# Performance work log

Measured on AMD Instinct MI355X. Metric: run time of the kernel, lower is better.

The kernel has to match this reference:

```python
import jax, jax.numpy as jnp
import numpy as np

K = 16
EPS = 1e-5

def _conv1x1(w, b, x):
    # w: [O, I], x: [B, I, N] -> [B, O, N]
    return jnp.einsum('oi,bin->bon', w, x) + b[None, :, None]

def _bn(g, be, m, v, x):
    # inference-mode batchnorm over channel dim of [B, C, N]
    inv = g / jnp.sqrt(v + EPS)
    return x * inv[None, :, None] + (be - m * inv)[None, :, None]

def setup_inputs() -> dict:
    key = jax.random.key(0)
    ks = jax.random.split(key, 16)
    B, C, N = 2, 128, 8192
    d = {}
    d['x'] = jax.random.normal(ks[0], (B, C, N), jnp.float32)
    d['xyz'] = jax.random.normal(ks[1], (B, N, 3), jnp.float32)
    def conv(k, o, i):
        k1, k2 = jax.random.split(k)
        s = 1.0 / np.sqrt(i)
        return (jax.random.uniform(k1, (o, i), jnp.float32, -s, s),
                jax.random.uniform(k2, (o,), jnp.float32, -s, s))
    def bn(k, c):
        return (jax.random.uniform(k, (c,), jnp.float32, 0.5, 1.5),
                jnp.zeros((c,), jnp.float32), jnp.zeros((c,), jnp.float32), jnp.ones((c,), jnp.float32))
    # boundary_net: 2C->C (bn,relu), C->C (bn,relu)
    d['bw1'], d['bb1'] = conv(ks[2], C, 2 * C)
    d['bn1g'], d['bn1b'], d['bn1m'], d['bn1v'] = bn(ks[3], C)
    d['bw2'], d['bb2'] = conv(ks[4], C, C)
    d['bn2g'], d['bn2b'], d['bn2m'], d['bn2v'] = bn(ks[5], C)
    # spatial_relation: 4->32 (bn,relu), 32->64
    d['sw1'], d['sb1'] = conv(ks[6], 32, 4)
    d['sbng'], d['sbnb'], d['sbnm'], d['sbnv'] = bn(ks[7], 32)
    d['sw2'], d['sb2'] = conv(ks[8], 64, 32)
    # attention: C+64 -> C//2 (bn,relu), C//2 -> C, sigmoid
    d['aw1'], d['ab1'] = conv(ks[9], C // 2, C + 64)
    d['abng'], d['abnb'], d['abnm'], d['abnv'] = bn(ks[10], C // 2)
    d['aw2'], d['ab2'] = conv(ks[11], C, C // 2)
    return d

def reference(x, xyz, bw1, bb1, bn1g, bn1b, bn1m, bn1v, bw2, bb2, bn2g, bn2b, bn2m, bn2v,
              sw1, sb1, sbng, sbnb, sbnm, sbnv, sw2, sb2,
              aw1, ab1, abng, abnb, abnm, abnv, aw2, ab2):
    B, C, N = x.shape
    # pairwise squared distances [B, N, N]
    xx = jnp.sum(xyz * xyz, axis=2)  # [B, N]
    dist = xx[:, :, None] + xx[:, None, :] - 2.0 * jnp.einsum('bnd,bmd->bnm', xyz, xyz)
    _, knn_idx = jax.lax.top_k(-dist, K)  # [B, N, K], K smallest distances
    # gather neighbor coords [B, N, K, 3]
    knn_xyz = jax.vmap(lambda p, i: p[i])(xyz, knn_idx)
    rel = knn_xyz - xyz[:, :, None, :]                  # [B, N, K, 3]
    rel_d = jnp.sqrt(jnp.sum(rel * rel, axis=-1))       # [B, N, K]
    mean_rel = jnp.mean(rel, axis=2).transpose(0, 2, 1)   # [B, 3, N]
    mean_d = jnp.mean(rel_d, axis=2)[:, None, :]           # [B, 1, N]
    spatial = jnp.concatenate([mean_rel, mean_d], axis=1)  # [B, 4, N]
    s = jax.nn.relu(_bn(sbng, sbnb, sbnm, sbnv, _conv1x1(sw1, sb1, spatial)))
    spatial_feat = _conv1x1(sw2, sb2, s)  # [B, 64, N]
    # gather neighbor features [B, C, N, K]
    knn_feat = jax.vmap(lambda xb, ib: xb[:, ib])(x, knn_idx)
    max_diff = jnp.max(knn_feat - x[:, :, :, None], axis=3)  # [B, C, N]
    bf = jnp.concatenate([x, max_diff], axis=1)  # [B, 2C, N]
    bf = jax.nn.relu(_bn(bn1g, bn1b, bn1m, bn1v, _conv1x1(bw1, bb1, bf)))
    boundary_feat = jax.nn.relu(_bn(bn2g, bn2b, bn2m, bn2v, _conv1x1(bw2, bb2, bf)))
    ai = jnp.concatenate([x, spatial_feat], axis=1)  # [B, C+64, N]
    a = jax.nn.relu(_bn(abng, abnb, abnm, abnv, _conv1x1(aw1, ab1, ai)))
    attn = jax.nn.sigmoid(_conv1x1(aw2, ab2, a))  # [B, C, N]
    return x + boundary_feat * attn
```

## Files before the change

### kernel.cpp

```cpp
#include <hip/hip_runtime.h>
#include <math.h>

#define NPTS  8192
#define NB    2
#define NTOT  (NPTS*NB)
#define GD    60
#define NCELL (GD*GD*GD)
#define TOTC  (NB*NCELL)
#define HCELL 0.2f
#define INVH  5.0f
#define ORGN  (-6.0f)
#define NN    8192
#define SCAN_CHUNK 1024
#define NBLK_SCAN  ((TOTC + SCAN_CHUNK - 1) / SCAN_CHUNK)
#define RMAX_GRID 4
#define RSTART    2
#define LIST_CAP 1024
#define SEL_CAP  1024

#define OFF_CNT     ((size_t)0)
#define OFF_OFFS    (OFF_CNT    + (size_t)TOTC*4)
#define OFF_CELLID  (OFF_OFFS   + (size_t)TOTC*4)
#define OFF_RANK    (OFF_CELLID + (size_t)NTOT*4)
#define OFF_SPOS    (OFF_RANK   + (size_t)NTOT*4)
#define OFF_KNN     (OFF_SPOS   + (size_t)NTOT*16)
#define OFF_SPATIAL (OFF_KNN    + (size_t)NTOT*16*4)
#define OFF_XT      (OFF_SPATIAL+ (size_t)NB*4*NPTS*4)
#define OFF_MD      (OFF_XT     + (size_t)NB*128*NPTS*4)
#define OFF_S1      (OFF_MD     + (size_t)NB*128*NPTS*4)
#define OFF_SF      (OFF_S1     + (size_t)NB*32*NPTS*4)
#define OFF_Y1      (OFF_SF     + (size_t)NB*64*NPTS*4)
#define OFF_Y2      (OFF_Y1     + (size_t)NB*128*NPTS*4)
#define OFF_A1      (OFF_Y2     + (size_t)NB*128*NPTS*4)
#define OFF_SC      (OFF_A1     + (size_t)NB*64*NPTS*4)
#define OFF_BSUM    (OFF_SC     + (size_t)1088*4)
#define OFF_BPRE    (OFF_BSUM   + (size_t)NBLK_SCAN*4)
#define OFF_RNG     (((OFF_BPRE + (size_t)NBLK_SCAN*4) + 15) & ~(size_t)15)

static __device__ __forceinline__ float sumsq3(float x, float y, float z) {
    return __fadd_rn(__fadd_rn(__fmul_rn(x, x), __fmul_rn(y, y)), __fmul_rn(z, z));
}
static __device__ __forceinline__ float pdist4(float qx, float qy, float qz, float qxx,
                                               float px, float py, float pz) {
    float pxx = sumsq3(px, py, pz);
    float dot = __fadd_rn(__fadd_rn(__fmul_rn(qx, px), __fmul_rn(qy, py)), __fmul_rn(qz, pz));
    return __fsub_rn(__fadd_rn(qxx, pxx), __fadd_rn(dot, dot));
}
static __device__ __forceinline__ unsigned fkey(float f) {
    unsigned b = __float_as_uint(f);
    return b ^ ((unsigned)(((int)b) >> 31) | 0x80000000u);
}
static __device__ __forceinline__ unsigned long long shflx64(unsigned long long v, int m) {
    unsigned lo = __shfl_xor((unsigned)v, m, 64);
    unsigned hi = __shfl_xor((unsigned)(v >> 32), m, 64);
    return ((unsigned long long)hi << 32) | lo;
}
static __device__ __forceinline__ int wave_scan_incl(int v, int lane) {
    #pragma unroll
    for (int d = 1; d < 64; d <<= 1) {
        int u = __shfl_up(v, d, 64);
        v += (lane >= d) ? u : 0;
    }
    return v;
}

__global__ void cell_build(const float* __restrict__ xyz, int* __restrict__ cnt,
                           int* __restrict__ cellid, int* __restrict__ rank) {
    int t = blockIdx.x * 256 + threadIdx.x;
    if (t >= NTOT) return;
    const float* p = xyz + (size_t)t * 3;
    float x = p[0], y = p[1], z = p[2];
    int cx = min(GD - 1, max(0, (int)floorf((x - ORGN) * INVH)));
    int cy = min(GD - 1, max(0, (int)floorf((y - ORGN) * INVH)));
    int cz = min(GD - 1, max(0, (int)floorf((z - ORGN) * INVH)));
    int gcell = (t >> 13) * NCELL + (cz * GD + cy) * GD + cx;
    rank[t] = atomicAdd(&cnt[gcell], 1);
    cellid[t] = gcell;
}

__global__ __launch_bounds__(256) void scan_sums(const int* __restrict__ cnt, int* __restrict__ bsum) {
    __shared__ int red[256];
    int blk = blockIdx.x, t = threadIdx.x;
    int i0 = blk * SCAN_CHUNK + t * 4;
    int s = 0;
    if (i0 + 3 < TOTC) {
        int4 v = *(const int4*)(cnt + i0);
        s = v.x + v.y + v.z + v.w;
    } else {
        for (int j = 0; j < 4; ++j) if (i0 + j < TOTC) s += cnt[i0 + j];
    }
    red[t] = s;
    __syncthreads();
    for (int d = 128; d > 0; d >>= 1) {
        if (t < d) red[t] += red[t + d];
        __syncthreads();
    }
    if (t == 0) bsum[blk] = red[0];
}

__global__ __launch_bounds__(512) void scan_top(const int* __restrict__ bsum, int* __restrict__ bpre) {
    __shared__ int ps[512];
    int t = threadIdx.x;
    int v = (t < NBLK_SCAN) ? bsum[t] : 0;
    ps[t] = v;
    __syncthreads();
    for (int d = 1; d < 512; d <<= 1) {
        int u = 0;
        if (t >= d) u = ps[t - d];
        __syncthreads();
        ps[t] += u;
        __syncthreads();
    }
    if (t < NBLK_SCAN) bpre[t] = ps[t] - v;
}

__global__ __launch_bounds__(256) void scan_write(const int* __restrict__ cnt, const int* __restrict__ bpre,
                                                  int* __restrict__ offs, int2* __restrict__ rng) {
    __shared__ int ps[256];
    int blk = blockIdx.x, t = threadIdx.x;
    int i0 = blk * SCAN_CHUNK + t * 4;
    int a = 0, b = 0, c = 0, d = 0;
    if (i0 + 3 < TOTC) {
        int4 v = *(const int4*)(cnt + i0);
        a = v.x; b = v.y; c = v.z; d = v.w;
    } else {
        if (i0 + 0 < TOTC) a = cnt[i0 + 0];
        if (i0 + 1 < TOTC) b = cnt[i0 + 1];
        if (i0 + 2 < TOTC) c = cnt[i0 + 2];
        if (i0 + 3 < TOTC) d = cnt[i0 + 3];
    }
    int s = a + b + c + d;
    ps[t] = s;
    __syncthreads();
    for (int dd = 1; dd < 256; dd <<= 1) {
        int u = 0;
        if (t >= dd) u = ps[t - dd];
        __syncthreads();
        ps[t] += u;
        __syncthreads();
    }
    int base = bpre[blk] + ps[t] - s;
    if (i0 + 3 < TOTC) {
        offs[i0 + 0] = base;
        offs[i0 + 1] = base + a;
        offs[i0 + 2] = base + a + b;
        offs[i0 + 3] = base + a + b + c;
        *(int4*)(rng + i0)     = make_int4(base, base + a, base + a, base + a + b);
        *(int4*)(rng + i0 + 2) = make_int4(base + a + b, base + a + b + c,
                                           base + a + b + c, base + s);
    } else {
        if (i0 + 0 < TOTC) { offs[i0 + 0] = base;             rng[i0 + 0] = make_int2(base, base + a); }
        if (i0 + 1 < TOTC) { offs[i0 + 1] = base + a;         rng[i0 + 1] = make_int2(base + a, base + a + b); }
        if (i0 + 2 < TOTC) { offs[i0 + 2] = base + a + b;     rng[i0 + 2] = make_int2(base + a + b, base + a + b + c); }
        if (i0 + 3 < TOTC) { offs[i0 + 3] = base + a + b + c; rng[i0 + 3] = make_int2(base + a + b + c, base + s); }
    }
}

__global__ void scatter_k(const float* __restrict__ xyz, const int* __restrict__ cellid,
                          const int* __restrict__ rank, const int* __restrict__ offs,
                          float4* __restrict__ spos) {
    int t = blockIdx.x * 256 + threadIdx.x;
    if (t >= NTOT) return;
    const float* p = xyz + (size_t)t * 3;
    float x = p[0], y = p[1], z = p[2];
    int pos = offs[cellid[t]] + rank[t];
    spos[pos] = make_float4(x, y, z, __int_as_float(t & (NPTS - 1)));
}

__global__ __launch_bounds__(64) void knn_kernel(const float4* __restrict__ spos,
                                                 const int2* __restrict__ rng,
                                                 int* __restrict__ knn,
                                                 float* __restrict__ spatial) {
    __shared__ __align__(16) char shraw[12288];
    int* lst = (int*)shraw;
    unsigned long long* sel = (unsigned long long*)(shraw + 4096);
    int lane = threadIdx.x;
    int bid  = blockIdx.x;
    int s = (bid & 7) * (NTOT / 8) + (bid >> 3);
    float4 q = spos[s];
    float qx = q.x, qy = q.y, qz = q.z;
    float qxx = sumsq3(qx, qy, qz);
    int b  = s >> 13;
    int nq = __float_as_int(q.w);
    int cx = min(GD - 1, max(0, (int)floorf((qx - ORGN) * INVH)));
    int cy = min(GD - 1, max(0, (int)floorf((qy - ORGN) * INVH)));
    int cz = min(GD - 1, max(0, (int)floorf((qz - ORGN) * INVH)));
    const int2* rg = rng + b * NCELL;

    float mlx = qx - (ORGN + (float)cx * HCELL);
    float mhx = (ORGN + (float)(cx + 1) * HCELL) - qx;
    float mly = qy - (ORGN + (float)cy * HCELL);
    float mhy = (ORGN + (float)(cy + 1) * HCELL) - qy;
    float mlz = qz - (ORGN + (float)cz * HCELL);
    float mhz = (ORGN + (float)(cz + 1) * HCELL) - qz;
    float margin0 = fminf(fminf(fminf(mlx, mhx), fminf(mly, mhy)), fminf(mlz, mhz));

    float mfin = margin0 + (float)(RMAX_GRID + 1) * HCELL;
    unsigned long long tkfin = (mfin > 0.f)
        ? ((unsigned long long)(fkey(mfin * mfin - 1e-4f) + 1u) << 27) : 0ULL;

    int tot = 0, ovf = 0;

    auto scan_runs = [&](int num, int start) {
        int rem = num, cur = start;
        for (;;) {
            int inc = wave_scan_incl(rem, lane);
            int ctot = __shfl(inc, 63, 64);
            if (ctot == 0) break;
            int excl = inc - rem;
            int space = LIST_CAP - excl;
            int take = min(rem, max(space, 0));
            for (int j = 0; j < take; ++j) lst[excl + j] = cur + j;
            rem -= take; cur += take;
            int n = min(ctot, LIST_CAP);
            asm volatile("s_waitcnt lgkmcnt(0)" ::: "memory");
            __builtin_amdgcn_sched_barrier(0);
            int sp_cur = (lane < n) ? lst[lane] : 0;
            float4 p_cur = spos[sp_cur];
            for (int t0 = 0; t0 < n; t0 += 64) {
                int tt = t0 + lane, tn = tt + 64;
                int sp_nx = (tn < n) ? lst[tn] : 0;
                float4 p_nx = spos[sp_nx];
                unsigned long long key = ~0ULL;
                if (tt < n) {
                    float d = pdist4(qx, qy, qz, qxx, p_cur.x, p_cur.y, p_cur.z);
                    key = ((unsigned long long)fkey(d) << 27)
                        | ((unsigned long long)(unsigned)__float_as_int(p_cur.w) << 14)
                        | (unsigned)sp_cur;
                }
                bool pass = (tt < n) && (key < tkfin);
                unsigned long long mk = __ballot(pass);
                int cnum = (int)__popcll(mk);
                if (tot + cnum > SEL_CAP) { ovf = 1; return; }
                if (pass) sel[tot + (int)__popcll(mk & ((1ULL << lane) - 1ULL))] = key;
                tot += cnum;
                sp_cur = sp_nx; p_cur = p_nx;
            }
            asm volatile("s_waitcnt lgkmcnt(0)" ::: "memory");
            __builtin_amdgcn_sched_barrier(0);
        }
    };

    int brute = (tkfin == 0ULL) ? 1 : 0;

    if (!brute) {
        int Lb = 2 * RSTART + 1;
        int nrows = Lb * Lb;
        int num = 0, start = 0;
        if (lane < nrows) {
            int dzr = lane / Lb - RSTART, dyr = lane % Lb - RSTART;
            int zc = cz + dzr, yc = cy + dyr;
            if ((unsigned)zc < GD && (unsigned)yc < GD) {
                int rowb = (zc * GD + yc) * GD;
                int xlo = max(cx - RSTART, 0), xhi = min(cx + RSTART, GD - 1);
                start = rg[rowb + xlo].x;
                num   = rg[rowb + xhi].y - start;
            }
        }
        scan_runs(num, start);
        if (ovf) brute = 1;
    }

    int R = RSTART;
    unsigned long long tkey_sel = ~0ULL;
    int cselq = 0;
    while (!brute) {
        float mR  = margin0 + (float)R * HCELL;
        float mR1 = mR - HCELL, mR2 = mR1 - HCELL;
        unsigned long long tk2 = (mR  > 0.f) ? ((unsigned long long)(fkey(mR  * mR  - 1e-4f) + 1u) << 27) : 0ULL;
        unsigned long long tk1 = (mR1 > 0.f) ? ((unsigned long long)(fkey(mR1 * mR1 - 1e-4f) + 1u) << 27) : 0ULL;
        unsigned long long tk0 = (mR2 > 0.f) ? ((unsigned long long)(fkey(mR2 * mR2 - 1e-4f) + 1u) << 27) : 0ULL;
        unsigned pk01 = 0; int c2 = 0;
        for (int t0 = 0; t0 < tot; t0 += 64) {
            int tt = t0 + lane;
            if (tt < tot) {
                unsigned long long v = sel[tt];
                pk01 += (v < tk0) ? 1u : 0u;
                pk01 += (v < tk1) ? 0x10000u : 0u;
                c2   += (v < tk2) ? 1 : 0;
            }
        }
        for (int o = 32; o > 0; o >>= 1) { pk01 += __shfl_xor(pk01, o, 64); c2 += __shfl_xor(c2, o, 64); }
        if (c2 >= 16) {
            int c0 = (int)(pk01 & 0xFFFFu), c1 = (int)(pk01 >> 16);
            if      (c0 >= 16) { tkey_sel = tk0; cselq = c0; }
            else if (c1 >= 16) { tkey_sel = tk1; cselq = c1; }
            else               { tkey_sel = tk2; cselq = c2; }
            break;
        }
        if (R >= RMAX_GRID) { brute = 1; break; }
        ++R;
        int Ls = 2 * R + 1;
        int P = Ls * Ls, P2 = (Ls - 2) * (Ls - 2);
        int nruns = P + P2;
        for (int r0 = 0; r0 < nruns && !ovf; r0 += 64) {
            int u = r0 + lane;
            int num = 0, start = 0;
            if (u < nruns) {
                int dzr, dyr, xlo, xhi;
                if (u < P) {
                    dzr = u / Ls - R; dyr = u % Ls - R;
                    bool outer = (dzr == -R || dzr == R || dyr == -R || dyr == R);
                    if (outer) { xlo = max(cx - R, 0); xhi = min(cx + R, GD - 1); }
                    else       { xlo = cx - R; xhi = cx - R; }
                } else {
                    int v = u - P; int L2 = Ls - 2;
                    dzr = v / L2 - (R - 1); dyr = v % L2 - (R - 1);
                    xlo = cx + R; xhi = cx + R;
                }
                int zc = cz + dzr, yc = cy + dyr;
                if ((unsigned)zc < GD && (unsigned)yc < GD && xlo >= 0 && xhi < GD) {
                    int rowb = (zc * GD + yc) * GD;
                    start = rg[rowb + xlo].x;
                    num   = rg[rowb + xhi].y - start;
                }
            }
            scan_runs(num, start);
        }
        if (ovf) brute = 1;
    }

    if (brute) {
        const float LADR[16] = {0.35f, 0.4725f, 0.637875f, 0.86113125f,
                                1.1625272f, 1.5694117f, 2.1187058f, 2.8602529f,
                                3.8613414f, 5.2128109f, 7.0372947f, 9.5003478f,
                                12.825470f, 17.314384f, 23.374418f, 31.555464f};
        int sbase = b << 13;
        int cc[16];
        #pragma unroll
        for (int k = 0; k < 16; ++k) cc[k] = 0;
        for (int i0 = 0; i0 < NPTS; i0 += 64) {
            float4 p = spos[sbase + i0 + lane];
            float d = pdist4(qx, qy, qz, qxx, p.x, p.y, p.z);
            #pragma unroll
            for (int k = 0; k < 16; ++k) cc[k] += (d < LADR[k] * LADR[k]) ? 1 : 0;
        }
        #pragma unroll
        for (int k = 0; k < 16; ++k)
            for (int o = 32; o > 0; o >>= 1) cc[k] += __shfl_xor(cc[k], o, 64);
        float Tq = LADR[15] * LADR[15]; int cL = cc[15];
        #pragma unroll
        for (int k = 14; k >= 0; --k) if (cc[k] >= 16) { Tq = LADR[k] * LADR[k]; cL = cc[k]; }
        if (cL <= SEL_CAP) {
            tot = 0;
            for (int i0 = 0; i0 < NPTS; i0 += 64) {
                int idx = sbase + i0 + lane;
                float4 p = spos[idx];
                float d = pdist4(qx, qy, qz, qxx, p.x, p.y, p.z);
                bool pass = (d < Tq);
                unsigned long long key = ((unsigned long long)fkey(d) << 27)
                                       | ((unsigned long long)(unsigned)__float_as_int(p.w) << 14)
                                       | (unsigned)idx;
                unsigned long long mk = __ballot(pass);
                if (pass) sel[tot + (int)__popcll(mk & ((1ULL << lane) - 1ULL))] = key;
                tot += (int)__popcll(mk);
            }
            tkey_sel = ~0ULL;
            cselq = tot;
        } else {
            unsigned long long* mybuf = ((unsigned long long*)shraw) + lane;
            unsigned long long minkey = ~0ULL, maxkey = 0;
            int nbuf = 0;
            for (int i = lane; i < NPTS; i += 64) {
                float4 p = spos[sbase + i];
                float d = pdist4(qx, qy, qz, qxx, p.x, p.y, p.z);
                unsigned long long key = ((unsigned long long)fkey(d) << 27)
                                       | ((unsigned long long)(unsigned)__float_as_int(p.w) << 14)
                                       | (unsigned)(sbase + i);
                if (nbuf < 16) {
                    mybuf[(size_t)nbuf * 64] = key;
                    ++nbuf;
                    minkey = (key < minkey) ? key : minkey;
                    maxkey = (key > maxkey) ? key : maxkey;
                } else if (key < maxkey) {
                    unsigned long long vmax = 0, v2 = 0;
                    int pmax = 0;
                    #pragma unroll
                    for (int j = 0; j < 16; ++j) {
                        unsigned long long v = mybuf[(size_t)j * 64];
                        if (v > vmax) { v2 = vmax; vmax = v; pmax = j; }
                        else if (v > v2) { v2 = v; }
                    }
                    mybuf[(size_t)pmax * 64] = key;
                    maxkey = (key > v2) ? key : v2;
                    minkey = (key < minkey) ? key : minkey;
                }
            }
            unsigned long long keep = ~0ULL;
            for (int k = 0; k < 16; ++k) {
                unsigned long long m = minkey;
                for (int o = 32; o > 0; o >>= 1) {
                    unsigned long long pv = shflx64(m, o);
                    m = (pv < m) ? pv : m;
                }
                unsigned long long bal = __ballot(minkey == m);
                int wl = __ffsll((long long)bal) - 1;
                if (lane == wl) {
                    int pos = 0;
                    for (int j = 0; j < nbuf; ++j) if (mybuf[(size_t)j * 64] == m) pos = j;
                    --nbuf;
                    mybuf[(size_t)pos * 64] = mybuf[(size_t)nbuf * 64];
                    unsigned long long nm = ~0ULL;
                    for (int j = 0; j < nbuf; ++j) {
                        unsigned long long v = mybuf[(size_t)j * 64];
                        nm = (v < nm) ? v : nm;
                    }
                    minkey = nm;
                }
                if (lane == k) keep = m;
            }
            float rx = 0.f, ry = 0.f, rz = 0.f, rd = 0.f;
            if (lane < 16) {
                int sp = (int)(keep & 0x3FFFu);
                int oi = (int)((keep >> 14) & 0x1FFFu);
                float4 p = spos[sp];
                rx = p.x - qx; ry = p.y - qy; rz = p.z - qz;
                rd = sqrtf(__fadd_rn(__fadd_rn(__fmul_rn(rx, rx), __fmul_rn(ry, ry)), __fmul_rn(rz, rz)));
                knn[(((size_t)b << 13) + nq) * 16 + lane] = oi;
            }
            for (int o = 8; o > 0; o >>= 1) {
                rx += __shfl_xor(rx, o, 64);
                ry += __shfl_xor(ry, o, 64);
                rz += __shfl_xor(rz, o, 64);
                rd += __shfl_xor(rd, o, 64);
            }
            if (lane == 0) {
                const float inv16 = 0.0625f;
                spatial[((size_t)b * 4 + 0) * NPTS + nq] = rx * inv16;
                spatial[((size_t)b * 4 + 1) * NPTS + nq] = ry * inv16;
                spatial[((size_t)b * 4 + 2) * NPTS + nq] = rz * inv16;
                spatial[((size_t)b * 4 + 3) * NPTS + nq] = rd * inv16;
            }
            return;
        }
    }

    asm volatile("s_waitcnt lgkmcnt(0)" ::: "memory");
    __builtin_amdgcn_sched_barrier(0);
    unsigned long long* sel2 = (unsigned long long*)shraw;
    const unsigned long long* src;
    int m;
    if (cselq <= 512) {
        int w = 0;
        for (int t0 = 0; t0 < tot; t0 += 64) {
            int tt = t0 + lane;
            unsigned long long v = (tt < tot) ? sel[tt] : ~0ULL;
            bool pass = (tt < tot) && (v < tkey_sel);
            unsigned long long mk = __ballot(pass);
            if (pass) sel2[w + (int)__popcll(mk & ((1ULL << lane) - 1ULL))] = v;
            w += (int)__popcll(mk);
        }
        asm volatile("s_waitcnt lgkmcnt(0)" ::: "memory");
        __builtin_amdgcn_sched_barrier(0);
        src = sel2; m = w;
    } else {
        src = sel; m = tot;
    }
    float rxs = 0.f, rys = 0.f, rzs = 0.f, rds = 0.f;
    for (int t0 = 0; t0 < m; t0 += 64) {
        int tt = t0 + lane;
        if (tt < m) {
            unsigned long long kt = src[tt];
            if (kt < tkey_sel) {
                int rr = 0;
                for (int j = 0; j < m; ++j) rr += (src[j] < kt) ? 1 : 0;
                if (rr < 16) {
                    int sp = (int)(kt & 0x3FFFu);
                    int oi = (int)((kt >> 14) & 0x1FFFu);
                    float4 p = spos[sp];
                    float dx = p.x - qx, dy = p.y - qy, dz = p.z - qz;
                    float dl = sqrtf(__fadd_rn(__fadd_rn(__fmul_rn(dx, dx), __fmul_rn(dy, dy)), __fmul_rn(dz, dz)));
                    knn[(((size_t)b << 13) + nq) * 16 + rr] = oi;
                    rxs += dx; rys += dy; rzs += dz; rds += dl;
                }
            }
        }
    }
    for (int o = 32; o > 0; o >>= 1) {
        rxs += __shfl_xor(rxs, o, 64);
        rys += __shfl_xor(rys, o, 64);
        rzs += __shfl_xor(rzs, o, 64);
        rds += __shfl_xor(rds, o, 64);
    }
    if (lane == 0) {
        const float inv16 = 0.0625f;
        spatial[((size_t)b * 4 + 0) * NPTS + nq] = rxs * inv16;
        spatial[((size_t)b * 4 + 1) * NPTS + nq] = rys * inv16;
        spatial[((size_t)b * 4 + 2) * NPTS + nq] = rzs * inv16;
        spatial[((size_t)b * 4 + 3) * NPTS + nq] = rds * inv16;
    }
}

__global__ void transpose_k(const float* __restrict__ x, float* __restrict__ xT) {
    __shared__ float tl[32][33];
    int b = blockIdx.z;
    int n0 = blockIdx.x * 32, c0 = blockIdx.y * 32;
    int tx = threadIdx.x, ty = threadIdx.y;
    const float* xb = x + (size_t)b * 128 * NN;
    float* xtb = xT + (size_t)b * NN * 128;
    for (int i = 0; i < 32; i += 8) tl[ty + i][tx] = xb[(size_t)(c0 + ty + i) * NN + n0 + tx];
    __syncthreads();
    for (int i = 0; i < 32; i += 8) xtb[(size_t)(n0 + ty + i) * 128 + c0 + tx] = tl[tx][ty + i];
}

__global__ __launch_bounds__(256) void md_k(const float* __restrict__ xT,
                                            const int* __restrict__ knn,
                                            float* __restrict__ md) {
    __shared__ int ki[8][16];
    __shared__ float smd[8][132];
    int b = blockIdx.y;
    int n0 = blockIdx.x * 8;
    int tid = threadIdx.x;
    if (tid < 128) ki[tid >> 4][tid & 15] = knn[(((size_t)b << 13) + n0 + (tid >> 4)) * 16 + (tid & 15)];
    __syncthreads();
    int nl = tid >> 5;
    int c4 = (tid & 31) * 4;
    const float* xb = xT + (size_t)b * NPTS * 128;
    float4 m = make_float4(-3.0e38f, -3.0e38f, -3.0e38f, -3.0e38f);
    #pragma unroll
    for (int k = 0; k < 16; ++k) {
        const float4 g = *(const float4*)(xb + (size_t)ki[nl][k] * 128 + c4);
        m.x = fmaxf(m.x, g.x); m.y = fmaxf(m.y, g.y); m.z = fmaxf(m.z, g.z); m.w = fmaxf(m.w, g.w);
    }
    const float4 own = *(const float4*)(xb + (size_t)(n0 + nl) * 128 + c4);
    m.x -= own.x; m.y -= own.y; m.z -= own.z; m.w -= own.w;
    *(float4*)(&smd[nl][c4]) = m;
    __syncthreads();
    for (int r = 0; r < 4; ++r) {
        int c = (tid >> 3) + 32 * r;
        int n2 = tid & 7;
        md[((size_t)b * 128 + c) * NN + n0 + n2] = smd[n2][c];
    }
}

__global__ void prep_k(const float* bb1, const float* g1, const float* be1, const float* m1, const float* v1,
                       const float* bb2, const float* g2, const float* be2, const float* m2, const float* v2,
                       const float* sb1, const float* gs,  const float* bes, const float* ms, const float* vs,
                       const float* sb2,
                       const float* ab1, const float* ga,  const float* bea, const float* ma, const float* va,
                       const float* ab2, float* sc) {
    int t = threadIdx.x;
    if (t < 128) {
        float i1 = g1[t] / sqrtf(v1[t] + 1e-5f);
        sc[t] = i1;        sc[128 + t] = bb1[t] * i1 + be1[t] - m1[t] * i1;
        float i2 = g2[t] / sqrtf(v2[t] + 1e-5f);
        sc[256 + t] = i2;  sc[384 + t] = bb2[t] * i2 + be2[t] - m2[t] * i2;
        sc[832 + t] = 1.0f; sc[960 + t] = ab2[t];
    }
    if (t < 32) {
        float is = gs[t] / sqrtf(vs[t] + 1e-5f);
        sc[512 + t] = is;  sc[544 + t] = sb1[t] * is + bes[t] - ms[t] * is;
    }
    if (t < 64) {
        sc[576 + t] = 1.0f; sc[640 + t] = sb2[t];
        float ia = ga[t] / sqrtf(va[t] + 1e-5f);
        sc[704 + t] = ia;  sc[768 + t] = ab1[t] * ia + bea[t] - ma[t] * ia;
    }
}

template <int O, int K, int TILE_N, int SPLIT, int ACT>
__global__ __launch_bounds__(256) void conv_bn(const float* __restrict__ srcA,
                                               const float* __restrict__ srcB,
                                               const float* __restrict__ W,
                                               const float* __restrict__ scale,
                                               const float* __restrict__ shift,
                                               float* __restrict__ out,
                                               const float* __restrict__ resx,
                                               const float* __restrict__ y2,
                                               float* __restrict__ dout) {
    constexpr int KC  = (K < 64) ? K : 64;
    constexpr int NT4 = TILE_N / 4;
    constexpr int O4  = O / 4;
    static_assert(NT4 * O4 == 256, "thread mapping");
    __shared__ float wT[KC][O + 4];
    __shared__ float inT[KC][TILE_N];
    int tid = threadIdx.x;
    int b = blockIdx.z;
    int n0 = blockIdx.x * TILE_N;
    int n_thr = tid % NT4;
    int o_thr = tid / NT4;
    float acc[4][4] = {{0.f, 0.f, 0.f, 0.f}, {0.f, 0.f, 0.f, 0.f}, {0.f, 0.f, 0.f, 0.f}, {0.f, 0.f, 0.f, 0.f}};

    for (int k0 = 0; k0 < K; k0 += KC) {
        for (int idx = tid; idx < KC * O; idx += 256) {
            int cc = idx % KC;
            int o  = idx / KC;
            wT[cc][o] = W[(size_t)o * K + k0 + cc];
        }
        for (int idx = tid; idx < KC * NT4; idx += 256) {
            int cc = idx / NT4;
            int nf = idx % NT4;
            int cg = k0 + cc;
            const float* src = (cg < SPLIT)
                ? (srcA + ((size_t)b * SPLIT + cg) * NN)
                : (srcB + ((size_t)b * (K - SPLIT) + (cg - SPLIT)) * NN);
            *(float4*)(&inT[cc][nf * 4]) = *(const float4*)(src + n0 + nf * 4);
        }
        __syncthreads();
        #pragma unroll 8
        for (int c = 0; c < KC; ++c) {
            float4 wv = *(const float4*)(&wT[c][o_thr * 4]);
            float4 iv = *(const float4*)(&inT[c][n_thr * 4]);
            acc[0][0] = fmaf(wv.x, iv.x, acc[0][0]); acc[0][1] = fmaf(wv.x, iv.y, acc[0][1]);
            acc[0][2] = fmaf(wv.x, iv.z, acc[0][2]); acc[0][3] = fmaf(wv.x, iv.w, acc[0][3]);
            acc[1][0] = fmaf(wv.y, iv.x, acc[1][0]); acc[1][1] = fmaf(wv.y, iv.y, acc[1][1]);
            acc[1][2] = fmaf(wv.y, iv.z, acc[1][2]); acc[1][3] = fmaf(wv.y, iv.w, acc[1][3]);
            acc[2][0] = fmaf(wv.z, iv.x, acc[2][0]); acc[2][1] = fmaf(wv.z, iv.y, acc[2][1]);
            acc[2][2] = fmaf(wv.z, iv.z, acc[2][2]); acc[2][3] = fmaf(wv.z, iv.w, acc[2][3]);
            acc[3][0] = fmaf(wv.w, iv.x, acc[3][0]); acc[3][1] = fmaf(wv.w, iv.y, acc[3][1]);
            acc[3][2] = fmaf(wv.w, iv.z, acc[3][2]); acc[3][3] = fmaf(wv.w, iv.w, acc[3][3]);
        }
        __syncthreads();
    }
    #pragma unroll
    for (int j = 0; j < 4; ++j) {
        int o = o_thr * 4 + j;
        float scv = scale[o], shv = shift[o];
        float4 v;
        v.x = fmaf(acc[j][0], scv, shv);
        v.y = fmaf(acc[j][1], scv, shv);
        v.z = fmaf(acc[j][2], scv, shv);
        v.w = fmaf(acc[j][3], scv, shv);
        size_t obase = ((size_t)b * O + o) * NN + n0 + n_thr * 4;
        if (ACT == 1) {
            v.x = fmaxf(v.x, 0.f); v.y = fmaxf(v.y, 0.f); v.z = fmaxf(v.z, 0.f); v.w = fmaxf(v.w, 0.f);
            *(float4*)(out + obase) = v;
        } else if (ACT == 2) {
            float4 xr = *(const float4*)(resx + obase);
            float4 yr = *(const float4*)(y2 + obase);
            v.x = xr.x + yr.x / (1.f + __expf(-v.x));
            v.y = xr.y + yr.y / (1.f + __expf(-v.y));
            v.z = xr.z + yr.z / (1.f + __expf(-v.z));
            v.w = xr.w + yr.w / (1.f + __expf(-v.w));
            *(float4*)(dout + obase) = v;
        } else {
            *(float4*)(out + obase) = v;
        }
    }
}

extern "C" void kernel_launch(void* const* d_in, const int* in_sizes, int n_in,
                              void* d_out, int out_size, void* d_ws, size_t ws_size,
                              hipStream_t stream) {
    (void)in_sizes; (void)n_in; (void)out_size; (void)ws_size;
    const float* x    = (const float*)d_in[0];
    const float* xyz  = (const float*)d_in[1];
    const float* bw1  = (const float*)d_in[2];
    const float* bb1  = (const float*)d_in[3];
    const float* bn1g = (const float*)d_in[4];
    const float* bn1b = (const float*)d_in[5];
    const float* bn1m = (const float*)d_in[6];
    const float* bn1v = (const float*)d_in[7];
    const float* bw2  = (const float*)d_in[8];
    const float* bb2  = (const float*)d_in[9];
    const float* bn2g = (const float*)d_in[10];
    const float* bn2b = (const float*)d_in[11];
    const float* bn2m = (const float*)d_in[12];
    const float* bn2v = (const float*)d_in[13];
    const float* sw1  = (const float*)d_in[14];
    const float* sb1  = (const float*)d_in[15];
    const float* sbng = (const float*)d_in[16];
    const float* sbnb = (const float*)d_in[17];
    const float* sbnm = (const float*)d_in[18];
    const float* sbnv = (const float*)d_in[19];
    const float* sw2  = (const float*)d_in[20];
    const float* sb2  = (const float*)d_in[21];
    const float* aw1  = (const float*)d_in[22];
    const float* ab1  = (const float*)d_in[23];
    const float* abng = (const float*)d_in[24];
    const float* abnb = (const float*)d_in[25];
    const float* abnm = (const float*)d_in[26];
    const float* abnv = (const float*)d_in[27];
    const float* aw2  = (const float*)d_in[28];
    const float* ab2  = (const float*)d_in[29];

    char* ws = (char*)d_ws;
    int*    cnt    = (int*)(ws + OFF_CNT);
    int*    offs   = (int*)(ws + OFF_OFFS);
    int*    cellid = (int*)(ws + OFF_CELLID);
    int*    rank   = (int*)(ws + OFF_RANK);
    float4* spos   = (float4*)(ws + OFF_SPOS);
    int*    knn    = (int*)(ws + OFF_KNN);
    float*  spat   = (float*)(ws + OFF_SPATIAL);
    float*  xT     = (float*)(ws + OFF_XT);
    float*  md     = (float*)(ws + OFF_MD);
    float*  s1b    = (float*)(ws + OFF_S1);
    float*  sfb    = (float*)(ws + OFF_SF);
    float*  y1b    = (float*)(ws + OFF_Y1);
    float*  y2b    = (float*)(ws + OFF_Y2);
    float*  a1b    = (float*)(ws + OFF_A1);
    float*  sc     = (float*)(ws + OFF_SC);
    int*    bsum   = (int*)(ws + OFF_BSUM);
    int*    bpre   = (int*)(ws + OFF_BPRE);
    int2*   rng    = (int2*)(ws + OFF_RNG);
    float*  dout   = (float*)d_out;

    hipMemsetAsync(cnt, 0, (size_t)TOTC * 4, stream);
    cell_build<<<dim3((NTOT + 255) / 256), 256, 0, stream>>>(xyz, cnt, cellid, rank);
    scan_sums<<<dim3(NBLK_SCAN), 256, 0, stream>>>(cnt, bsum);
    scan_top<<<dim3(1), 512, 0, stream>>>(bsum, bpre);
    scan_write<<<dim3(NBLK_SCAN), 256, 0, stream>>>(cnt, bpre, offs, rng);
    scatter_k<<<dim3((NTOT + 255) / 256), 256, 0, stream>>>(xyz, cellid, rank, offs, spos);
    knn_kernel<<<dim3(NTOT), 64, 0, stream>>>(spos, rng, knn, spat);
    transpose_k<<<dim3(NPTS / 32, 128 / 32, NB), dim3(32, 8), 0, stream>>>(x, xT);
    md_k<<<dim3(NPTS / 8, NB), 256, 0, stream>>>(xT, knn, md);
    prep_k<<<1, 128, 0, stream>>>(bb1, bn1g, bn1b, bn1m, bn1v,
                                  bb2, bn2g, bn2b, bn2m, bn2v,
                                  sb1, sbng, sbnb, sbnm, sbnv,
                                  sb2,
                                  ab1, abng, abnb, abnm, abnv,
                                  ab2, sc);
    conv_bn<32, 4, 128, 4, 1><<<dim3(NPTS / 128, 1, NB), 256, 0, stream>>>(
        spat, spat, sw1, sc + 512, sc + 544, s1b, nullptr, nullptr, nullptr);
    conv_bn<64, 32, 64, 32, 0><<<dim3(NPTS / 64, 1, NB), 256, 0, stream>>>(
        s1b, s1b, sw2, sc + 576, sc + 640, sfb, nullptr, nullptr, nullptr);
    conv_bn<128, 256, 32, 128, 1><<<dim3(NPTS / 32, 1, NB), 256, 0, stream>>>(
        x, md, bw1, sc + 0, sc + 128, y1b, nullptr, nullptr, nullptr);
    conv_bn<128, 128, 32, 128, 1><<<dim3(NPTS / 32, 1, NB), 256, 0, stream>>>(
        y1b, y1b, bw2, sc + 256, sc + 384, y2b, nullptr, nullptr, nullptr);
    conv_bn<64, 192, 64, 128, 1><<<dim3(NPTS / 64, 1, NB), 256, 0, stream>>>(
        x, sfb, aw1, sc + 704, sc + 768, a1b, nullptr, nullptr, nullptr);
    conv_bn<128, 64, 32, 64, 2><<<dim3(NPTS / 32, 1, NB), 256, 0, stream>>>(
        a1b, a1b, aw2, sc + 832, sc + 960, dout, x, y2b, dout);
}
```

Baseline: 336.2 us.

## Replace incremental shell-grown kNN grid search with clipped-sphere ball scans

The kNN kernel no longer grows the search cube shell by shell from R=2 to 4 with a full count at every step. It now scans a sphere-clipped set of cell rows at radius 2 and, if too few candidates pass, rescans once at radius 4 before the brute-force fallback. Candidate indices come from a binary search over per-row prefix sums with shuffles, replacing the LDS index list, and the next batch is prefetched. This is meant to cut cell visits, LDS traffic and loop overhead, at the cost of a full rescan for hard queries and shuffle-heavy index decoding.

```diff
diff --git a/kernel.cpp b/kernel.cpp
--- a/kernel.cpp
+++ b/kernel.cpp
@@ -13,9 +13,8 @@
 #define NN    8192
 #define SCAN_CHUNK 1024
 #define NBLK_SCAN  ((TOTC + SCAN_CHUNK - 1) / SCAN_CHUNK)
-#define RMAX_GRID 4
 #define RSTART    2
-#define LIST_CAP 1024
+#define RESC      4
 #define SEL_CAP  1024
 
 #define OFF_CNT     ((size_t)0)
@@ -63,6 +62,9 @@
     }
     return v;
 }
+static __device__ __forceinline__ unsigned long long tkmake(float m) {
+    return ((unsigned long long)(fkey(__fsub_rn(__fmul_rn(m, m), 1e-4f)) + 1u)) << 27;
+}
 
 __global__ void cell_build(const float* __restrict__ xyz, int* __restrict__ cnt,
                            int* __restrict__ cellid, int* __restrict__ rank) {
@@ -171,9 +173,8 @@
                                                  const int2* __restrict__ rng,
                                                  int* __restrict__ knn,
                                                  float* __restrict__ spatial) {
-    __shared__ __align__(16) char shraw[12288];
-    int* lst = (int*)shraw;
-    unsigned long long* sel = (unsigned long long*)(shraw + 4096);
+    __shared__ __align__(16) unsigned long long sel[SEL_CAP];
+    __shared__ __align__(16) unsigned long long sel2[512];
     int lane = threadIdx.x;
     int bid  = blockIdx.x;
     int s = (bid & 7) * (NTOT / 8) + (bid >> 3);
@@ -195,132 +196,120 @@
     float mhz = (ORGN + (float)(cz + 1) * HCELL) - qz;
     float margin0 = fminf(fminf(fminf(mlx, mhx), fminf(mly, mhy)), fminf(mlz, mhz));
 
-    float mfin = margin0 + (float)(RMAX_GRID + 1) * HCELL;
-    unsigned long long tkfin = (mfin > 0.f)
-        ? ((unsigned long long)(fkey(mfin * mfin - 1e-4f) + 1u) << 27) : 0ULL;
-
     int tot = 0, ovf = 0;
 
-    auto scan_runs = [&](int num, int start) {
-        int rem = num, cur = start;
-        for (;;) {
-            int inc = wave_scan_incl(rem, lane);
+    auto scan_ball = [&](int RB, float mfin, unsigned long long tkfin) {
+        if (mfin <= 0.f) return;
+        float mfin2 = mfin * mfin;
+        int L = 2 * RB + 1, nrows = L * L;
+        for (int r0 = 0; r0 < nrows; r0 += 64) {
+            int nr = min(64, nrows - r0);
+            int rr = r0 + lane;
+            int num = 0, start = 0;
+            if (rr < nrows) {
+                int dzr = rr / L - RB, dyr = rr % L - RB;
+                int zc = cz + dzr, yc = cy + dyr;
+                if ((unsigned)zc < GD && (unsigned)yc < GD) {
+                    float ylo = ORGN + (float)yc * HCELL;
+                    float zlo = ORGN + (float)zc * HCELL;
+                    float dyl = fmaxf(fmaxf(ylo - qy, qy - (ylo + HCELL)), 0.f);
+                    float dzl = fmaxf(fmaxf(zlo - qz, qz - (zlo + HCELL)), 0.f);
+                    float rem = mfin2 - dyl * dyl - dzl * dzl;
+                    if (rem > -1e-4f) {
+                        float xh = sqrtf(fmaxf(rem, 0.f)) + 1e-3f;
+                        int xlo = max(0, (int)floorf((qx - xh - ORGN) * INVH));
+                        int xhi = min(GD - 1, (int)floorf((qx + xh - ORGN) * INVH));
+                        if (xlo <= xhi) {
+                            int rowb = (zc * GD + yc) * GD;
+                            start = rg[rowb + xlo].x;
+                            num   = rg[rowb + xhi].y - start;
+                        }
+                    }
+                }
+            }
+            int inc = wave_scan_incl(num, lane);
             int ctot = __shfl(inc, 63, 64);
-            if (ctot == 0) break;
-            int excl = inc - rem;
-            int space = LIST_CAP - excl;
-            int take = min(rem, max(space, 0));
-            for (int j = 0; j < take; ++j) lst[excl + j] = cur + j;
-            rem -= take; cur += take;
-            int n = min(ctot, LIST_CAP);
-            asm volatile("s_waitcnt lgkmcnt(0)" ::: "memory");
-            __builtin_amdgcn_sched_barrier(0);
-            int sp_cur = (lane < n) ? lst[lane] : 0;
-            float4 p_cur = spos[sp_cur];
-            for (int t0 = 0; t0 < n; t0 += 64) {
-                int tt = t0 + lane, tn = tt + 64;
-                int sp_nx = (tn < n) ? lst[tn] : 0;
-                float4 p_nx = spos[sp_nx];
-                unsigned long long key = ~0ULL;
-                if (tt < n) {
-                    float d = pdist4(qx, qy, qz, qxx, p_cur.x, p_cur.y, p_cur.z);
-                    key = ((unsigned long long)fkey(d) << 27)
-                        | ((unsigned long long)(unsigned)__float_as_int(p_cur.w) << 14)
-                        | (unsigned)sp_cur;
+            if (ctot == 0) continue;
+            int excl = inc - num;
+            auto eg = [&](int base, int& sv, float4& pv, bool& vld) {
+                int t = base + lane;
+                vld = t < ctot;
+                int tc = vld ? t : (ctot - 1);
+                int lo = 0, hi = nr - 1;
+                #pragma unroll
+                for (int st = 0; st < 6; ++st) {
+                    int mid = (lo + hi + 1) >> 1;
+                    int e = __shfl(excl, mid, 64);
+                    bool g = (e <= tc);
+                    lo = g ? mid : lo;
+                    hi = g ? hi : (mid - 1);
                 }
-                bool pass = (tt < n) && (key < tkfin);
+                sv = __shfl(start, lo, 64) + (tc - __shfl(excl, lo, 64));
+                pv = spos[sv];
+            };
+            int s0; float4 p0; bool v0;
+            eg(0, s0, p0, v0);
+            for (int base = 0; base < ctot; base += 64) {
+                int s1 = 0; float4 p1 = p0; bool v1 = false;
+                if (base + 64 < ctot) eg(base + 64, s1, p1, v1);
+                float d = pdist4(qx, qy, qz, qxx, p0.x, p0.y, p0.z);
+                unsigned long long key = ((unsigned long long)fkey(d) << 27)
+                                       | ((unsigned long long)(unsigned)__float_as_int(p0.w) << 14)
+                                       | (unsigned)s0;
+                bool pass = v0 && (key < tkfin);
                 unsigned long long mk = __ballot(pass);
                 int cnum = (int)__popcll(mk);
                 if (tot + cnum > SEL_CAP) { ovf = 1; return; }
                 if (pass) sel[tot + (int)__popcll(mk & ((1ULL << lane) - 1ULL))] = key;
                 tot += cnum;
-                sp_cur = sp_nx; p_cur = p_nx;
-            }
-            asm volatile("s_waitcnt lgkmcnt(0)" ::: "memory");
-            __builtin_amdgcn_sched_barrier(0);
+                s0 = s1; p0 = p1; v0 = v1;
+            }
         }
     };
 
-    int brute = (tkfin == 0ULL) ? 1 : 0;
-
-    if (!brute) {
-        int Lb = 2 * RSTART + 1;
-        int nrows = Lb * Lb;
-        int num = 0, start = 0;
-        if (lane < nrows) {
-            int dzr = lane / Lb - RSTART, dyr = lane % Lb - RSTART;
-            int zc = cz + dzr, yc = cy + dyr;
-            if ((unsigned)zc < GD && (unsigned)yc < GD) {
-                int rowb = (zc * GD + yc) * GD;
-                int xlo = max(cx - RSTART, 0), xhi = min(cx + RSTART, GD - 1);
-                start = rg[rowb + xlo].x;
-                num   = rg[rowb + xhi].y - start;
-            }
-        }
-        scan_runs(num, start);
-        if (ovf) brute = 1;
-    }
-
-    int R = RSTART;
-    unsigned long long tkey_sel = ~0ULL;
-    int cselq = 0;
-    while (!brute) {
-        float mR  = margin0 + (float)R * HCELL;
-        float mR1 = mR - HCELL, mR2 = mR1 - HCELL;
-        unsigned long long tk2 = (mR  > 0.f) ? ((unsigned long long)(fkey(mR  * mR  - 1e-4f) + 1u) << 27) : 0ULL;
-        unsigned long long tk1 = (mR1 > 0.f) ? ((unsigned long long)(fkey(mR1 * mR1 - 1e-4f) + 1u) << 27) : 0ULL;
-        unsigned long long tk0 = (mR2 > 0.f) ? ((unsigned long long)(fkey(mR2 * mR2 - 1e-4f) + 1u) << 27) : 0ULL;
-        unsigned pk01 = 0; int c2 = 0;
+    auto count_below = [&](unsigned long long tk) {
+        int c = 0;
         for (int t0 = 0; t0 < tot; t0 += 64) {
             int tt = t0 + lane;
-            if (tt < tot) {
-                unsigned long long v = sel[tt];
-                pk01 += (v < tk0) ? 1u : 0u;
-                pk01 += (v < tk1) ? 0x10000u : 0u;
-                c2   += (v < tk2) ? 1 : 0;
-            }
-        }
-        for (int o = 32; o > 0; o >>= 1) { pk01 += __shfl_xor(pk01, o, 64); c2 += __shfl_xor(c2, o, 64); }
-        if (c2 >= 16) {
-            int c0 = (int)(pk01 & 0xFFFFu), c1 = (int)(pk01 >> 16);
-            if      (c0 >= 16) { tkey_sel = tk0; cselq = c0; }
-            else if (c1 >= 16) { tkey_sel = tk1; cselq = c1; }
-            else               { tkey_sel = tk2; cselq = c2; }
-            break;
-        }
-        if (R >= RMAX_GRID) { brute = 1; break; }
-        ++R;
-        int Ls = 2 * R + 1;
-        int P = Ls * Ls, P2 = (Ls - 2) * (Ls - 2);
-        int nruns = P + P2;
-        for (int r0 = 0; r0 < nruns && !ovf; r0 += 64) {
-            int u = r0 + lane;
-            int num = 0, start = 0;
-            if (u < nruns) {
-                int dzr, dyr, xlo, xhi;
-                if (u < P) {
-                    dzr = u / Ls - R; dyr = u % Ls - R;
-                    bool outer = (dzr == -R || dzr == R || dyr == -R || dyr == R);
-                    if (outer) { xlo = max(cx - R, 0); xhi = min(cx + R, GD - 1); }
-                    else       { xlo = cx - R; xhi = cx - R; }
-                } else {
-                    int v = u - P; int L2 = Ls - 2;
-                    dzr = v / L2 - (R - 1); dyr = v % L2 - (R - 1);
-                    xlo = cx + R; xhi = cx + R;
-                }
-                int zc = cz + dzr, yc = cy + dyr;
-                if ((unsigned)zc < GD && (unsigned)yc < GD && xlo >= 0 && xhi < GD) {
-                    int rowb = (zc * GD + yc) * GD;
-                    start = rg[rowb + xlo].x;
-                    num   = rg[rowb + xhi].y - start;
-                }
-            }
-            scan_runs(num, start);
-        }
-        if (ovf) brute = 1;
-    }
-
-    if (brute) {
+            if (tt < tot) c += (sel[tt] < tk) ? 1 : 0;
+        }
+        for (int o = 32; o > 0; o >>= 1) c += __shfl_xor(c, o, 64);
+        return c;
+    };
+
+    float mfin1 = margin0 + (float)RSTART * HCELL;
+    unsigned long long tkf1 = (mfin1 > 0.f) ? tkmake(mfin1) : 0ULL;
+    if (tkf1) scan_ball(RSTART, mfin1, tkf1);
+
+    unsigned long long tkey_sel = ~0ULL;
+    int csel = 0;
+    bool have = false;
+    if (!ovf && tot >= 16) {
+        float mA = margin0 + 1.0f * HCELL;
+        if (mA > 0.f) {
+            unsigned long long tkA = tkmake(mA);
+            int cA = count_below(tkA);
+            if (cA >= 16) { tkey_sel = tkA; csel = cA; have = true; }
+        }
+        if (!have) { tkey_sel = ~0ULL; csel = tot; have = true; }
+    }
+    if (!have && !ovf) {
+        tot = 0;
+        float mfin4 = margin0 + (float)RESC * HCELL;
+        unsigned long long tkf4 = (mfin4 > 0.f) ? tkmake(mfin4) : 0ULL;
+        if (tkf4) scan_ball(RESC, mfin4, tkf4);
+        if (!ovf && tot >= 16) {
+            float mB = margin0 + (float)(RESC - 1) * HCELL;
+            if (mB > 0.f) {
+                unsigned long long tkB = tkmake(mB);
+                int cB = count_below(tkB);
+                if (cB >= 16) { tkey_sel = tkB; csel = cB; have = true; }
+            }
+            if (!have) { tkey_sel = ~0ULL; csel = tot; have = true; }
+        }
+    }
+
+    if (!have) {
         const float LADR[16] = {0.35f, 0.4725f, 0.637875f, 0.86113125f,
                                 1.1625272f, 1.5694117f, 2.1187058f, 2.8602529f,
                                 3.8613414f, 5.2128109f, 7.0372947f, 9.5003478f,
@@ -356,9 +345,9 @@
                 tot += (int)__popcll(mk);
             }
             tkey_sel = ~0ULL;
-            cselq = tot;
+            csel = tot;
         } else {
-            unsigned long long* mybuf = ((unsigned long long*)shraw) + lane;
+            unsigned long long* mybuf = sel + lane;
             unsigned long long minkey = ~0ULL, maxkey = 0;
             int nbuf = 0;
             for (int i = lane; i < NPTS; i += 64) {
@@ -435,12 +424,9 @@
         }
     }
 
-    asm volatile("s_waitcnt lgkmcnt(0)" ::: "memory");
-    __builtin_amdgcn_sched_barrier(0);
-    unsigned long long* sel2 = (unsigned long long*)shraw;
-    const unsigned long long* src;
-    int m;
-    if (cselq <= 512) {
+    const unsigned long long* src = sel;
+    int m = tot;
+    if (tkey_sel != ~0ULL && csel <= 512) {
         int w = 0;
         for (int t0 = 0; t0 < tot; t0 += 64) {
             int tt = t0 + lane;
@@ -453,8 +439,7 @@
         asm volatile("s_waitcnt lgkmcnt(0)" ::: "memory");
         __builtin_amdgcn_sched_barrier(0);
         src = sel2; m = w;
-    } else {
-        src = sel; m = tot;
+        tkey_sel = ~0ULL;
     }
     float rxs = 0.f, rys = 0.f, rzs = 0.f, rds = 0.f;
     for (int t0 = 0; t0 < m; t0 += 64) {
```

Measured after the change: 326.0 us. 3.0% less time.
